# Optimization experiments

Measured on AMD Instinct MI355X. Metric: run time of the kernel, lower is better.

The kernel has to match this reference:

```python
import jax, jax.numpy as jnp
from jax import lax
import numpy as np

INPUT_SIZE = 4
HIDDEN = 64
PROJ = 52


def setup_inputs() -> dict:
    key = jax.random.key(0)
    ks = jax.random.split(key, 6)
    k = 1.0 / np.sqrt(HIDDEN)  # PyTorch LSTM init range
    u = lambda kk, shape: jax.random.uniform(kk, shape, jnp.float32, -k, k)
    return {
        "x": jax.random.normal(ks[0], (4096, 512, INPUT_SIZE), jnp.float32),
        "W_ih": u(ks[1], (4 * HIDDEN, INPUT_SIZE)),   # gates [i,f,g,o]
        "W_hh": u(ks[2], (4 * HIDDEN, PROJ)),          # recurrent acts on projected h
        "b_ih": u(ks[3], (4 * HIDDEN,)),
        "b_hh": u(ks[4], (4 * HIDDEN,)),
        "W_hr": u(ks[5], (PROJ, HIDDEN)),              # projection h = W_hr @ (o*tanh(c))
    }


def reference(x, W_ih, W_hh, b_ih, b_hh, W_hr):
    B = x.shape[0]
    b = b_ih + b_hh
    xT = jnp.swapaxes(x, 0, 1)  # [T, B, input]

    def step(carry, xt):
        h, c = carry  # h: [B, PROJ], c: [B, HIDDEN]
        gates = xt @ W_ih.T + h @ W_hh.T + b  # [B, 4H]
        i, f, g, o = jnp.split(gates, 4, axis=-1)
        i = jax.nn.sigmoid(i)
        f = jax.nn.sigmoid(f)
        g = jnp.tanh(g)
        o = jax.nn.sigmoid(o)
        c = f * c + i * g
        h = (o * jnp.tanh(c)) @ W_hr.T  # projected hidden state
        return (h, c), None

    h0 = jnp.zeros((B, PROJ), x.dtype)
    c0 = jnp.zeros((B, HIDDEN), x.dtype)
    (h_last, _), _ = lax.scan(step, (h0, c0), xT)
    return h_last  # [B, PROJ] == r_out[:, -1, :]
```

## Files before the change

### kernel.cpp

```cpp
#include <hip/hip_runtime.h>


#define T_STEPS 512
#define HID 64
#define NPROJ 52
#define NBATCH 16
#define ROWB 136
#define LOG2E 1.44269504088896340736f

typedef _Float16 half8 __attribute__((ext_vector_type(8)));
typedef float f32x4 __attribute__((ext_vector_type(4)));

__device__ __forceinline__ float exp2_f(float x) {
#if __has_builtin(__builtin_amdgcn_exp2f)
    return __builtin_amdgcn_exp2f(x);
#else
    return exp2f(x);
#endif
}
__device__ __forceinline__ float rcp_f(float x) {
    return __builtin_amdgcn_rcpf(x);
}

__global__ __launch_bounds__(256, 1)
void lstmp_kernel(const float* __restrict__ x,
                  const float* __restrict__ Wih,
                  const float* __restrict__ Whh,
                  const float* __restrict__ bih,
                  const float* __restrict__ bhh,
                  const float* __restrict__ Whr,
                  float* __restrict__ out)
{
    __shared__ unsigned long long dlds[2 * NBATCH * ROWB / 8];

    const int lane = threadIdx.x & 63;
    const int wave = threadIdx.x >> 6;
    const int quad = lane >> 4;
    const int col  = lane & 15;

    half8 aG[4][2];
    const int hid = wave * 16 + col;
#pragma unroll
    for (int g = 0; g < 4; ++g) {
        const float scale = (g == 2) ? (2.0f * LOG2E) : LOG2E;
        const int row = g * HID + hid;
#pragma unroll
        for (int ch = 0; ch < 2; ++ch) {
#pragma unroll
            for (int j = 0; j < 8; ++j) {
                const int k = ch * 32 + quad * 8 + j;
                float v;
                if (k < NPROJ)      v = Whh[row * NPROJ + k];
                else if (k < 56)    v = Wih[row * 4 + (k - NPROJ)];
                else if (k == 56)   v = bih[row] + bhh[row];
                else                v = 0.0f;
                aG[g][ch][j] = (_Float16)(v * scale);
            }
        }
    }

    half8 aP[4][2];
#pragma unroll
    for (int tt = 0; tt < 4; ++tt) {
        const int p = ((tt >> 1) * 32) + ((col >> 2) * 8) + ((tt & 1) * 4) + (col & 3);
#pragma unroll
        for (int ch = 0; ch < 2; ++ch) {
#pragma unroll
            for (int j = 0; j < 8; ++j) {
                const int k = ch * 32 + quad * 8 + j;
                aP[tt][ch][j] = (_Float16)((p < NPROJ) ? Whr[p * HID + k] : 0.0f);
            }
        }
    }

    const float4* xp = (const float4*)x + (size_t)blockIdx.x * NBATCH * T_STEPS;
    const float4 x0 = xp[(size_t)col * T_STEPS + 0];
    float4 xv = xp[(size_t)col * T_STEPS + 1];

    half8 b0, b1;
#pragma unroll
    for (int j = 0; j < 8; ++j) { b0[j] = (_Float16)0.0f; b1[j] = (_Float16)0.0f; }
    if (quad == 2) {
        b1[4] = (_Float16)x0.x; b1[5] = (_Float16)x0.y;
        b1[6] = (_Float16)x0.z; b1[7] = (_Float16)x0.w;
    }
    if (quad == 3) {
        b1[0] = (_Float16)1.0f;
    }

    float cacc[4] = {0.0f, 0.0f, 0.0f, 0.0f};
    f32x4 hp[4];

    const int dwoff = col * ROWB + wave * 32 + quad * 8;
    const int drbase = col * ROWB + quad * 16;

#pragma unroll 1
    for (int t = 0; t < T_STEPS; ++t) {
        f32x4 ai = {0.f,0.f,0.f,0.f}, af_ = {0.f,0.f,0.f,0.f};
        f32x4 ag_ = {0.f,0.f,0.f,0.f}, ao_ = {0.f,0.f,0.f,0.f};
        ai  = __builtin_amdgcn_mfma_f32_16x16x32_f16(aG[0][0], b0, ai,  0, 0, 0);
        af_ = __builtin_amdgcn_mfma_f32_16x16x32_f16(aG[1][0], b0, af_, 0, 0, 0);
        ag_ = __builtin_amdgcn_mfma_f32_16x16x32_f16(aG[2][0], b0, ag_, 0, 0, 0);
        ao_ = __builtin_amdgcn_mfma_f32_16x16x32_f16(aG[3][0], b0, ao_, 0, 0, 0);
        ai  = __builtin_amdgcn_mfma_f32_16x16x32_f16(aG[0][1], b1, ai,  0, 0, 0);
        af_ = __builtin_amdgcn_mfma_f32_16x16x32_f16(aG[1][1], b1, af_, 0, 0, 0);
        ag_ = __builtin_amdgcn_mfma_f32_16x16x32_f16(aG[2][1], b1, ag_, 0, 0, 0);
        ao_ = __builtin_amdgcn_mfma_f32_16x16x32_f16(aG[3][1], b1, ao_, 0, 0, 0);

        char* dbuf = (char*)dlds + (t & 1) * (NBATCH * ROWB);
        union { _Float16 h[4]; unsigned long long q; } du;
#pragma unroll
        for (int r = 0; r < 4; ++r) {
            const float iv = rcp_f(1.0f + exp2_f(-ai[r]));
            const float fv = rcp_f(1.0f + exp2_f(-af_[r]));
            const float ov = rcp_f(1.0f + exp2_f(-ao_[r]));
            const float gs = fmaf(-4.0f * LOG2E, rcp_f(1.0f + exp2_f(ag_[r])),
                                  2.0f * LOG2E);
            const float cn = fmaf(fv, cacc[r], iv * gs);
            cacc[r] = cn;
            const float th = fmaf(-2.0f, rcp_f(1.0f + exp2_f(cn)), 1.0f);
            du.h[r] = (_Float16)(ov * th);
        }
        *(unsigned long long*)(dbuf + dwoff) = du.q;
        __syncthreads();

        half8 bd0, bd1;
        {
            const char* p0 = dbuf + drbase;
            union { unsigned long long q[2]; half8 h; } u0, u1;
            u0.q[0] = *(const unsigned long long*)(p0);
            u0.q[1] = *(const unsigned long long*)(p0 + 8);
            u1.q[0] = *(const unsigned long long*)(p0 + 64);
            u1.q[1] = *(const unsigned long long*)(p0 + 72);
            bd0 = u0.h; bd1 = u1.h;
        }

#pragma unroll
        for (int tt = 0; tt < 4; ++tt) {
            f32x4 acc = {0.f, 0.f, 0.f, 0.f};
            acc = __builtin_amdgcn_mfma_f32_16x16x32_f16(aP[tt][0], bd0, acc, 0, 0, 0);
            acc = __builtin_amdgcn_mfma_f32_16x16x32_f16(aP[tt][1], bd1, acc, 0, 0, 0);
            hp[tt] = acc;
        }

#pragma unroll
        for (int j = 0; j < 4; ++j) {
            b0[j]     = (_Float16)hp[0][j];
            b0[4 + j] = (_Float16)hp[1][j];
            b1[j]     = (_Float16)hp[2][j];
            b1[4 + j] = (_Float16)hp[3][j];
        }
        if (quad == 2) {
            b1[4] = (_Float16)xv.x; b1[5] = (_Float16)xv.y;
            b1[6] = (_Float16)xv.z; b1[7] = (_Float16)xv.w;
        }
        if (quad == 3) {
            b1[0] = (_Float16)1.0f;
        }

        const int tn = (t + 2 < T_STEPS) ? (t + 2) : (T_STEPS - 1);
        xv = xp[(size_t)col * T_STEPS + tn];
    }

    if (wave == 0) {
        const size_t bg = (size_t)blockIdx.x * NBATCH + col;
        float* o = out + bg * NPROJ;
#pragma unroll
        for (int tt = 0; tt < 4; ++tt) {
            const int pb = ((tt >> 1) * 32) + (quad * 8) + ((tt & 1) * 4);
#pragma unroll
            for (int r = 0; r < 4; ++r) {
                const int p = pb + r;
                if (p < NPROJ) o[p] = hp[tt][r];
            }
        }
    }
}

extern "C" void kernel_launch(void* const* d_in, const int* in_sizes, int n_in,
                              void* d_out, int out_size, void* d_ws, size_t ws_size,
                              hipStream_t stream) {
    const float* x   = (const float*)d_in[0];
    const float* Wih = (const float*)d_in[1];
    const float* Whh = (const float*)d_in[2];
    const float* bih = (const float*)d_in[3];
    const float* bhh = (const float*)d_in[4];
    const float* Whr = (const float*)d_in[5];
    float* out = (float*)d_out;

    dim3 grid(4096 / NBATCH);
    dim3 block(256);
    lstmp_kernel<<<grid, block, 0, stream>>>(x, Wih, Whh, bih, bhh, Whr, out);
}
```

Before: 341.3 us.

## Halve batch per block and split gate activations across lane halves via bpermute

Each block now handles 8 batch rows instead of 16, doubling the grid to 512 blocks and allowing 2 blocks per CU. The MFMA B columns 8-15 duplicate columns 0-7. Lanes in the upper half take rows 2-3 of the accumulators through ds_bpermute, so each lane evaluates 2 transcendental activation sets instead of 4. This is meant to shorten the serial per-step activation latency and raise occupancy so two independent recurrences can interleave. The cost is extra permute instructions, MFMA work on duplicated columns, LDS zero-init, and a staggered s_sleep on odd blocks.

```diff
diff --git a/kernel.cpp b/kernel.cpp
--- a/kernel.cpp
+++ b/kernel.cpp
@@ -4,7 +4,7 @@
 #define T_STEPS 512
 #define HID 64
 #define NPROJ 52
-#define NBATCH 16
+#define NBATCH 8
 #define ROWB 136
 #define LOG2E 1.44269504088896340736f
 
@@ -21,8 +21,11 @@
 __device__ __forceinline__ float rcp_f(float x) {
     return __builtin_amdgcn_rcpf(x);
 }
-
-__global__ __launch_bounds__(256, 1)
+__device__ __forceinline__ float bperm_f(int addrB, float v) {
+    return __int_as_float(__builtin_amdgcn_ds_bpermute(addrB, __float_as_int(v)));
+}
+
+__global__ __launch_bounds__(256, 2)
 void lstmp_kernel(const float* __restrict__ x,
                   const float* __restrict__ Wih,
                   const float* __restrict__ Whh,
@@ -31,12 +34,14 @@
                   const float* __restrict__ Whr,
                   float* __restrict__ out)
 {
-    __shared__ unsigned long long dlds[2 * NBATCH * ROWB / 8];
+    __shared__ unsigned long long dlds[2 * 16 * ROWB / 8];
 
     const int lane = threadIdx.x & 63;
     const int wave = threadIdx.x >> 6;
     const int quad = lane >> 4;
     const int col  = lane & 15;
+    const bool lowhalf = (col < 8);
+    const int srcB = (lane & ~8) << 2;
 
     half8 aG[4][2];
     const int hid = wave * 16 + col;
@@ -73,9 +78,15 @@
         }
     }
 
+    {
+        unsigned* ldw = (unsigned*)dlds;
+        const int tot = (int)(sizeof(dlds) / 4);
+        for (int i = threadIdx.x; i < tot; i += 256) ldw[i] = 0u;
+    }
+
     const float4* xp = (const float4*)x + (size_t)blockIdx.x * NBATCH * T_STEPS;
-    const float4 x0 = xp[(size_t)col * T_STEPS + 0];
-    float4 xv = xp[(size_t)col * T_STEPS + 1];
+    const float4 x0 = xp[(size_t)(col & 7) * T_STEPS + 0];
+    float4 xv = xp[(size_t)(col & 7) * T_STEPS + 1];
 
     half8 b0, b1;
 #pragma unroll
@@ -88,11 +99,15 @@
         b1[0] = (_Float16)1.0f;
     }
 
-    float cacc[4] = {0.0f, 0.0f, 0.0f, 0.0f};
+    float cacc[2] = {0.0f, 0.0f};
     f32x4 hp[4];
 
-    const int dwoff = col * ROWB + wave * 32 + quad * 8;
+    const int dwoff = (col & 7) * ROWB + (16 * wave + quad * 4 + (lowhalf ? 0 : 2)) * 2;
     const int drbase = col * ROWB + quad * 16;
+
+    __syncthreads();
+
+    if (blockIdx.x & 1) __builtin_amdgcn_s_sleep(16);
 
 #pragma unroll 1
     for (int t = 0; t < T_STEPS; ++t) {
@@ -107,21 +122,37 @@
         ag_ = __builtin_amdgcn_mfma_f32_16x16x32_f16(aG[2][1], b1, ag_, 0, 0, 0);
         ao_ = __builtin_amdgcn_mfma_f32_16x16x32_f16(aG[3][1], b1, ao_, 0, 0, 0);
 
-        char* dbuf = (char*)dlds + (t & 1) * (NBATCH * ROWB);
-        union { _Float16 h[4]; unsigned long long q; } du;
-#pragma unroll
-        for (int r = 0; r < 4; ++r) {
-            const float iv = rcp_f(1.0f + exp2_f(-ai[r]));
-            const float fv = rcp_f(1.0f + exp2_f(-af_[r]));
-            const float ov = rcp_f(1.0f + exp2_f(-ao_[r]));
-            const float gs = fmaf(-4.0f * LOG2E, rcp_f(1.0f + exp2_f(ag_[r])),
-                                  2.0f * LOG2E);
-            const float cn = fmaf(fv, cacc[r], iv * gs);
-            cacc[r] = cn;
-            const float th = fmaf(-2.0f, rcp_f(1.0f + exp2_f(cn)), 1.0f);
-            du.h[r] = (_Float16)(ov * th);
-        }
-        *(unsigned long long*)(dbuf + dwoff) = du.q;
+        float yi0, yi1, yf0, yf1, yg0, yg1, yo0, yo1;
+        {
+            const float ti2 = bperm_f(srcB, ai[2]),  ti3 = bperm_f(srcB, ai[3]);
+            const float tf2 = bperm_f(srcB, af_[2]), tf3 = bperm_f(srcB, af_[3]);
+            const float tg2 = bperm_f(srcB, ag_[2]), tg3 = bperm_f(srcB, ag_[3]);
+            const float to2 = bperm_f(srcB, ao_[2]), to3 = bperm_f(srcB, ao_[3]);
+            yi0 = lowhalf ? ai[0]  : ti2;  yi1 = lowhalf ? ai[1]  : ti3;
+            yf0 = lowhalf ? af_[0] : tf2;  yf1 = lowhalf ? af_[1] : tf3;
+            yg0 = lowhalf ? ag_[0] : tg2;  yg1 = lowhalf ? ag_[1] : tg3;
+            yo0 = lowhalf ? ao_[0] : to2;  yo1 = lowhalf ? ao_[1] : to3;
+        }
+
+        char* dbuf = (char*)dlds + (t & 1) * (16 * ROWB);
+        union { _Float16 h[2]; unsigned w; } du;
+        {
+            const float yi[2] = {yi0, yi1}, yf[2] = {yf0, yf1};
+            const float yg[2] = {yg0, yg1}, yo[2] = {yo0, yo1};
+#pragma unroll
+            for (int u = 0; u < 2; ++u) {
+                const float iv = rcp_f(1.0f + exp2_f(-yi[u]));
+                const float fv = rcp_f(1.0f + exp2_f(-yf[u]));
+                const float ov = rcp_f(1.0f + exp2_f(-yo[u]));
+                const float gs = fmaf(-4.0f * LOG2E, rcp_f(1.0f + exp2_f(yg[u])),
+                                      2.0f * LOG2E);
+                const float cn = fmaf(fv, cacc[u], iv * gs);
+                cacc[u] = cn;
+                const float th = fmaf(-2.0f, rcp_f(1.0f + exp2_f(cn)), 1.0f);
+                du.h[u] = (_Float16)(ov * th);
+            }
+        }
+        *(unsigned*)(dbuf + dwoff) = du.w;
         __syncthreads();
 
         half8 bd0, bd1;
@@ -159,10 +190,10 @@
         }
 
         const int tn = (t + 2 < T_STEPS) ? (t + 2) : (T_STEPS - 1);
-        xv = xp[(size_t)col * T_STEPS + tn];
-    }
-
-    if (wave == 0) {
+        xv = xp[(size_t)(col & 7) * T_STEPS + tn];
+    }
+
+    if (wave == 0 && lowhalf) {
         const size_t bg = (size_t)blockIdx.x * NBATCH + col;
         float* o = out + bg * NPROJ;
 #pragma unroll
```

Result: slower. 416.8 us (+22.1%).

## Fold projection into recurrent weights to remove per-step projection MFMAs

Applied to the files above, without the earlier changes.

Precomputes M = W_hh·W_hr so the recurrence works directly on the unprojected o*tanh(c) vector read from LDS. This removes the per-step projection matmul and its fp16 conversion chain from the serial critical path. The projection is applied once at the end, and the x and bias contribution is issued as a separate MFMA before the LDS read so it can overlap. In exchange the recurrent K grows from 52 to 64, and precision may drift slightly because the fused weights are rounded to fp16.

```diff
diff --git a/kernel.cpp b/kernel.cpp
--- a/kernel.cpp
+++ b/kernel.cpp
@@ -6,6 +6,7 @@
 #define NPROJ 52
 #define NBATCH 16
 #define ROWB 136
+#define DBYTES (NBATCH * ROWB)
 #define LOG2E 1.44269504088896340736f
 
 typedef _Float16 half8 __attribute__((ext_vector_type(8)));
@@ -31,83 +32,127 @@
                   const float* __restrict__ Whr,
                   float* __restrict__ out)
 {
-    __shared__ unsigned long long dlds[2 * NBATCH * ROWB / 8];
+    __shared__ char dlds[2 * DBYTES];
 
     const int lane = threadIdx.x & 63;
     const int wave = threadIdx.x >> 6;
     const int quad = lane >> 4;
     const int col  = lane & 15;
 
-    half8 aG[4][2];
+    {
+        unsigned* ldw = (unsigned*)dlds;
+        const int tot = (int)(2 * DBYTES / 4);
+        for (int i = threadIdx.x; i < tot; i += 256) ldw[i] = 0u;
+    }
+
     const int hid = wave * 16 + col;
+    float macc[4][16];
+#pragma unroll
+    for (int g = 0; g < 4; ++g)
+#pragma unroll
+        for (int kk = 0; kk < 16; ++kk) macc[g][kk] = 0.0f;
+
+    for (int p = 0; p < NPROJ; ++p) {
+        float wv[4];
+#pragma unroll
+        for (int g = 0; g < 4; ++g) wv[g] = Whh[(g * HID + hid) * NPROJ + p];
+        const float* wr = Whr + p * HID + quad * 8;
+        const float4 r0 = *(const float4*)(wr);
+        const float4 r1 = *(const float4*)(wr + 4);
+        const float4 r2 = *(const float4*)(wr + 32);
+        const float4 r3 = *(const float4*)(wr + 36);
+        const float rk[16] = {r0.x, r0.y, r0.z, r0.w, r1.x, r1.y, r1.z, r1.w,
+                              r2.x, r2.y, r2.z, r2.w, r3.x, r3.y, r3.z, r3.w};
+#pragma unroll
+        for (int g = 0; g < 4; ++g)
+#pragma unroll
+            for (int kk = 0; kk < 16; ++kk) macc[g][kk] = fmaf(wv[g], rk[kk], macc[g][kk]);
+    }
+
+    half8 aM[4][2];
+    half8 aXB[4];
 #pragma unroll
     for (int g = 0; g < 4; ++g) {
         const float scale = (g == 2) ? (2.0f * LOG2E) : LOG2E;
+#pragma unroll
+        for (int ch = 0; ch < 2; ++ch)
+#pragma unroll
+            for (int j = 0; j < 8; ++j)
+                aM[g][ch][j] = (_Float16)(macc[g][ch * 8 + j] * scale);
         const int row = g * HID + hid;
 #pragma unroll
-        for (int ch = 0; ch < 2; ++ch) {
-#pragma unroll
-            for (int j = 0; j < 8; ++j) {
-                const int k = ch * 32 + quad * 8 + j;
-                float v;
-                if (k < NPROJ)      v = Whh[row * NPROJ + k];
-                else if (k < 56)    v = Wih[row * 4 + (k - NPROJ)];
-                else if (k == 56)   v = bih[row] + bhh[row];
-                else                v = 0.0f;
-                aG[g][ch][j] = (_Float16)(v * scale);
-            }
-        }
-    }
-
-    half8 aP[4][2];
-#pragma unroll
-    for (int tt = 0; tt < 4; ++tt) {
-        const int p = ((tt >> 1) * 32) + ((col >> 2) * 8) + ((tt & 1) * 4) + (col & 3);
-#pragma unroll
-        for (int ch = 0; ch < 2; ++ch) {
-#pragma unroll
-            for (int j = 0; j < 8; ++j) {
-                const int k = ch * 32 + quad * 8 + j;
-                aP[tt][ch][j] = (_Float16)((p < NPROJ) ? Whr[p * HID + k] : 0.0f);
-            }
+        for (int j = 0; j < 8; ++j) {
+            const int k = quad * 8 + j;
+            float v = 0.0f;
+            if (k < 4)       v = Wih[row * 4 + k];
+            else if (k == 4) v = bih[row] + bhh[row];
+            aXB[g][j] = (_Float16)(v * scale);
         }
     }
 
     const float4* xp = (const float4*)x + (size_t)blockIdx.x * NBATCH * T_STEPS;
-    const float4 x0 = xp[(size_t)col * T_STEPS + 0];
+    const float4 xq0 = xp[(size_t)col * T_STEPS + 0];
     float4 xv = xp[(size_t)col * T_STEPS + 1];
 
-    half8 b0, b1;
-#pragma unroll
-    for (int j = 0; j < 8; ++j) { b0[j] = (_Float16)0.0f; b1[j] = (_Float16)0.0f; }
-    if (quad == 2) {
-        b1[4] = (_Float16)x0.x; b1[5] = (_Float16)x0.y;
-        b1[6] = (_Float16)x0.z; b1[7] = (_Float16)x0.w;
-    }
-    if (quad == 3) {
-        b1[0] = (_Float16)1.0f;
+    half8 bx;
+#pragma unroll
+    for (int j = 0; j < 8; ++j) bx[j] = (_Float16)0.0f;
+    if (quad == 0) {
+        bx[0] = (_Float16)xq0.x; bx[1] = (_Float16)xq0.y;
+        bx[2] = (_Float16)xq0.z; bx[3] = (_Float16)xq0.w;
+        bx[4] = (_Float16)1.0f;
     }
 
     float cacc[4] = {0.0f, 0.0f, 0.0f, 0.0f};
-    f32x4 hp[4];
-
-    const int dwoff = col * ROWB + wave * 32 + quad * 8;
+
+    const int dwoff  = col * ROWB + wave * 32 + quad * 8;
     const int drbase = col * ROWB + quad * 16;
+
+    __syncthreads();
 
 #pragma unroll 1
     for (int t = 0; t < T_STEPS; ++t) {
+        const char* rbuf = dlds + (t & 1) * DBYTES;
+        char* wbuf = dlds + ((t + 1) & 1) * DBYTES;
+
         f32x4 ai = {0.f,0.f,0.f,0.f}, af_ = {0.f,0.f,0.f,0.f};
         f32x4 ag_ = {0.f,0.f,0.f,0.f}, ao_ = {0.f,0.f,0.f,0.f};
-        ai  = __builtin_amdgcn_mfma_f32_16x16x32_f16(aG[0][0], b0, ai,  0, 0, 0);
-        af_ = __builtin_amdgcn_mfma_f32_16x16x32_f16(aG[1][0], b0, af_, 0, 0, 0);
-        ag_ = __builtin_amdgcn_mfma_f32_16x16x32_f16(aG[2][0], b0, ag_, 0, 0, 0);
-        ao_ = __builtin_amdgcn_mfma_f32_16x16x32_f16(aG[3][0], b0, ao_, 0, 0, 0);
-        ai  = __builtin_amdgcn_mfma_f32_16x16x32_f16(aG[0][1], b1, ai,  0, 0, 0);
-        af_ = __builtin_amdgcn_mfma_f32_16x16x32_f16(aG[1][1], b1, af_, 0, 0, 0);
-        ag_ = __builtin_amdgcn_mfma_f32_16x16x32_f16(aG[2][1], b1, ag_, 0, 0, 0);
-        ao_ = __builtin_amdgcn_mfma_f32_16x16x32_f16(aG[3][1], b1, ao_, 0, 0, 0);
-
-        char* dbuf = (char*)dlds + (t & 1) * (NBATCH * ROWB);
+        ai  = __builtin_amdgcn_mfma_f32_16x16x32_f16(aXB[0], bx, ai,  0, 0, 0);
+        af_ = __builtin_amdgcn_mfma_f32_16x16x32_f16(aXB[1], bx, af_, 0, 0, 0);
+        ag_ = __builtin_amdgcn_mfma_f32_16x16x32_f16(aXB[2], bx, ag_, 0, 0, 0);
+        ao_ = __builtin_amdgcn_mfma_f32_16x16x32_f16(aXB[3], bx, ao_, 0, 0, 0);
+
+        half8 bd0, bd1;
+        {
+            const char* p0 = rbuf + drbase;
+            union { unsigned long long q[2]; half8 h; } u0, u1;
+            u0.q[0] = *(const unsigned long long*)(p0);
+            u0.q[1] = *(const unsigned long long*)(p0 + 8);
+            u1.q[0] = *(const unsigned long long*)(p0 + 64);
+            u1.q[1] = *(const unsigned long long*)(p0 + 72);
+            bd0 = u0.h; bd1 = u1.h;
+        }
+
+        half8 bxn;
+#pragma unroll
+        for (int j = 0; j < 8; ++j) bxn[j] = (_Float16)0.0f;
+        if (quad == 0) {
+            bxn[0] = (_Float16)xv.x; bxn[1] = (_Float16)xv.y;
+            bxn[2] = (_Float16)xv.z; bxn[3] = (_Float16)xv.w;
+            bxn[4] = (_Float16)1.0f;
+        }
+        const int tn = (t + 2 < T_STEPS) ? (t + 2) : (T_STEPS - 1);
+        const float4 xnew = xp[(size_t)col * T_STEPS + tn];
+
+        ai  = __builtin_amdgcn_mfma_f32_16x16x32_f16(aM[0][0], bd0, ai,  0, 0, 0);
+        af_ = __builtin_amdgcn_mfma_f32_16x16x32_f16(aM[1][0], bd0, af_, 0, 0, 0);
+        ag_ = __builtin_amdgcn_mfma_f32_16x16x32_f16(aM[2][0], bd0, ag_, 0, 0, 0);
+        ao_ = __builtin_amdgcn_mfma_f32_16x16x32_f16(aM[3][0], bd0, ao_, 0, 0, 0);
+        ai  = __builtin_amdgcn_mfma_f32_16x16x32_f16(aM[0][1], bd1, ai,  0, 0, 0);
+        af_ = __builtin_amdgcn_mfma_f32_16x16x32_f16(aM[1][1], bd1, af_, 0, 0, 0);
+        ag_ = __builtin_amdgcn_mfma_f32_16x16x32_f16(aM[2][1], bd1, ag_, 0, 0, 0);
+        ao_ = __builtin_amdgcn_mfma_f32_16x16x32_f16(aM[3][1], bd1, ao_, 0, 0, 0);
+
         union { _Float16 h[4]; unsigned long long q; } du;
 #pragma unroll
         for (int r = 0; r < 4; ++r) {
@@ -121,59 +166,44 @@
             const float th = fmaf(-2.0f, rcp_f(1.0f + exp2_f(cn)), 1.0f);
             du.h[r] = (_Float16)(ov * th);
         }
-        *(unsigned long long*)(dbuf + dwoff) = du.q;
+        *(unsigned long long*)(wbuf + dwoff) = du.q;
+
+        bx = bxn;
+        xv = xnew;
         __syncthreads();
-
-        half8 bd0, bd1;
-        {
-            const char* p0 = dbuf + drbase;
-            union { unsigned long long q[2]; half8 h; } u0, u1;
-            u0.q[0] = *(const unsigned long long*)(p0);
-            u0.q[1] = *(const unsigned long long*)(p0 + 8);
-            u1.q[0] = *(const unsigned long long*)(p0 + 64);
-            u1.q[1] = *(const unsigned long long*)(p0 + 72);
-            bd0 = u0.h; bd1 = u1.h;
-        }
-
-#pragma unroll
-        for (int tt = 0; tt < 4; ++tt) {
-            f32x4 acc = {0.f, 0.f, 0.f, 0.f};
-            acc = __builtin_amdgcn_mfma_f32_16x16x32_f16(aP[tt][0], bd0, acc, 0, 0, 0);
-            acc = __builtin_amdgcn_mfma_f32_16x16x32_f16(aP[tt][1], bd1, acc, 0, 0, 0);
-            hp[tt] = acc;
-        }
-
-#pragma unroll
-        for (int j = 0; j < 4; ++j) {
-            b0[j]     = (_Float16)hp[0][j];
-            b0[4 + j] = (_Float16)hp[1][j];
-            b1[j]     = (_Float16)hp[2][j];
-            b1[4 + j] = (_Float16)hp[3][j];
-        }
-        if (quad == 2) {
-            b1[4] = (_Float16)xv.x; b1[5] = (_Float16)xv.y;
-            b1[6] = (_Float16)xv.z; b1[7] = (_Float16)xv.w;
-        }
-        if (quad == 3) {
-            b1[0] = (_Float16)1.0f;
-        }
-
-        const int tn = (t + 2 < T_STEPS) ? (t + 2) : (T_STEPS - 1);
-        xv = xp[(size_t)col * T_STEPS + tn];
-    }
-
-    if (wave == 0) {
-        const size_t bg = (size_t)blockIdx.x * NBATCH + col;
-        float* o = out + bg * NPROJ;
-#pragma unroll
-        for (int tt = 0; tt < 4; ++tt) {
-            const int pb = ((tt >> 1) * 32) + (quad * 8) + ((tt & 1) * 4);
-#pragma unroll
-            for (int r = 0; r < 4; ++r) {
-                const int p = pb + r;
-                if (p < NPROJ) o[p] = hp[tt][r];
-            }
-        }
+    }
+
+    half8 aP[2];
+    const int prow = wave * 16 + col;
+#pragma unroll
+    for (int ch = 0; ch < 2; ++ch)
+#pragma unroll
+        for (int j = 0; j < 8; ++j) {
+            const int k = ch * 32 + quad * 8 + j;
+            aP[ch][j] = (_Float16)((prow < NPROJ) ? Whr[prow * HID + k] : 0.0f);
+        }
+
+    half8 bd0, bd1;
+    {
+        const char* p0 = dlds + 0 * DBYTES + drbase;
+        union { unsigned long long q[2]; half8 h; } u0, u1;
+        u0.q[0] = *(const unsigned long long*)(p0);
+        u0.q[1] = *(const unsigned long long*)(p0 + 8);
+        u1.q[0] = *(const unsigned long long*)(p0 + 64);
+        u1.q[1] = *(const unsigned long long*)(p0 + 72);
+        bd0 = u0.h; bd1 = u1.h;
+    }
+    f32x4 hf = {0.f, 0.f, 0.f, 0.f};
+    hf = __builtin_amdgcn_mfma_f32_16x16x32_f16(aP[0], bd0, hf, 0, 0, 0);
+    hf = __builtin_amdgcn_mfma_f32_16x16x32_f16(aP[1], bd1, hf, 0, 0, 0);
+
+    const size_t bg = (size_t)blockIdx.x * NBATCH + col;
+    float* o = out + bg * NPROJ;
+    const int p0 = wave * 16 + quad * 4;
+#pragma unroll
+    for (int r = 0; r < 4; ++r) {
+        const int p = p0 + r;
+        if (p < NPROJ) o[p] = hf[r];
     }
 }
 
```

After: 310.6 us. 1.1x faster.
